# Optimization experiments

Measured on AMD Instinct MI355X. Metric: run time of the kernel, lower is better.

## Reference

```python
import jax, jax.numpy as jnp
import numpy as np

N_NODES = 100000
HIDDEN = 128
N_EDGES = 1600000


def setup_inputs() -> dict:
    key = jax.random.key(0)
    k_z, k_e, k_w1, k_b1, k_w2, k_b2 = jax.random.split(key, 6)
    z = jax.random.normal(k_z, (N_NODES, HIDDEN), dtype=jnp.float32)
    edge_index = jax.random.randint(k_e, (2, N_EDGES), 0, N_NODES, dtype=jnp.int64)
    # torch.nn.Linear default init: U(-1/sqrt(fan_in), 1/sqrt(fan_in))
    lim1 = 1.0 / np.sqrt(2 * HIDDEN)
    W1 = jax.random.uniform(k_w1, (2 * HIDDEN, HIDDEN), minval=-lim1, maxval=lim1, dtype=jnp.float32)
    b1 = jax.random.uniform(k_b1, (HIDDEN,), minval=-lim1, maxval=lim1, dtype=jnp.float32)
    lim2 = 1.0 / np.sqrt(HIDDEN)
    W2 = jax.random.uniform(k_w2, (HIDDEN, 1), minval=-lim2, maxval=lim2, dtype=jnp.float32)
    b2 = jax.random.uniform(k_b2, (1,), minval=-lim2, maxval=lim2, dtype=jnp.float32)
    return {"z": z, "edge_index": edge_index, "W1": W1, "b1": b1, "W2": W2, "b2": b2}


def reference(z, edge_index, W1, b1, W2, b2):
    src = edge_index[0]
    dst = edge_index[1]
    # gather node pairs -> concat: [E, 2H]
    edge_feat = jnp.concatenate([z[src], z[dst]], axis=1)
    h = jax.nn.relu(edge_feat @ W1 + b1)  # [E, H]
    score = h @ W2 + b2                   # [E, 1]
    return score
```

## Files before the change

kernel.cpp:

```cpp
#include <hip/hip_runtime.h>
#include <hip/hip_bf16.h>
#include <stdint.h>

#define HIDDEN 128

typedef __attribute__((ext_vector_type(8))) short bf16x8;
typedef __attribute__((ext_vector_type(16))) float f32x16;

static __device__ __forceinline__ unsigned short f2bf(float f) {
    union { float f; uint32_t u; } v; v.f = f;
    uint32_t u = v.u;
    uint32_t r = (u + 0x7fffu + ((u >> 16) & 1u)) >> 16;
    return (unsigned short)r;
}
static __device__ __forceinline__ float bf_lo(uint32_t p) {
    union { uint32_t u; float f; } v; v.u = p << 16; return v.f;
}
static __device__ __forceinline__ float bf_hi(uint32_t p) {
    union { uint32_t u; float f; } v; v.u = p & 0xffff0000u; return v.f;
}
static __device__ __forceinline__ bf16x8 pack8(float4 a, float4 b) {
    bf16x8 r;
    r[0] = (short)f2bf(a.x); r[1] = (short)f2bf(a.y);
    r[2] = (short)f2bf(a.z); r[3] = (short)f2bf(a.w);
    r[4] = (short)f2bf(b.x); r[5] = (short)f2bf(b.y);
    r[6] = (short)f2bf(b.z); r[7] = (short)f2bf(b.w);
    return r;
}


struct ZBuf { float4 a[8], b[8]; };

static __device__ __forceinline__ void load_z(ZBuf& zb, const float* __restrict__ z,
                                              int ng, int nl, int hi, int n_nodes) {
    int node = ng * 32 + nl;
    node = (node < n_nodes) ? node : (n_nodes - 1);
    const float* zrow = z + (size_t)node * HIDDEN;
    #pragma unroll
    for (int ks = 0; ks < 8; ++ks) {
        zb.a[ks] = *reinterpret_cast<const float4*>(zrow + ks * 16 + hi * 8);
        zb.b[ks] = *reinterpret_cast<const float4*>(zrow + ks * 16 + hi * 8 + 4);
    }
}

static __device__ __forceinline__ void compute_store(
    const ZBuf& zb, const bf16x8 (&wf)[2][8], const f32x16 (&binit)[2],
    unsigned short* __restrict__ UV, int ng, int nl, int hi, int w, int n_nodes)
{
    bf16x8 zf[8];
    #pragma unroll
    for (int ks = 0; ks < 8; ++ks) zf[ks] = pack8(zb.a[ks], zb.b[ks]);

    f32x16 acc0 = binit[0];
    f32x16 acc1 = binit[1];
    #pragma unroll
    for (int ks = 0; ks < 8; ++ks) {
        acc0 = __builtin_amdgcn_mfma_f32_32x32x16_bf16(wf[0][ks], zf[ks], acc0, 0, 0, 0);
        acc1 = __builtin_amdgcn_mfma_f32_32x32x16_bf16(wf[1][ks], zf[ks], acc1, 0, 0, 0);
    }

    const int node = ng * 32 + nl;
    if (node < n_nodes) {
        unsigned short* orow = UV + (size_t)node * 256;
        #pragma unroll
        for (int g = 0; g < 4; ++g) {
            ushort4 s0, s1;
            s0.x = f2bf(acc0[4 * g + 0]); s0.y = f2bf(acc0[4 * g + 1]);
            s0.z = f2bf(acc0[4 * g + 2]); s0.w = f2bf(acc0[4 * g + 3]);
            s1.x = f2bf(acc1[4 * g + 0]); s1.y = f2bf(acc1[4 * g + 1]);
            s1.z = f2bf(acc1[4 * g + 2]); s1.w = f2bf(acc1[4 * g + 3]);
            *reinterpret_cast<ushort4*>(orow + w * 64 + g * 8 + hi * 4) = s0;
            *reinterpret_cast<ushort4*>(orow + w * 64 + 32 + g * 8 + hi * 4) = s1;
        }
    }
}

__global__ __launch_bounds__(256) void precompute_mfma32(
    const float* __restrict__ z, const float* __restrict__ W1,
    const float* __restrict__ b1,
    unsigned short* __restrict__ UV, int n_nodes, int n_groups)
{
    const int lane = threadIdx.x & 63;
    const int w = threadIdx.x >> 6;
    const int nl = lane & 31;
    const int hi = lane >> 5;

    bf16x8 wf[2][8];
    #pragma unroll
    for (int cg = 0; cg < 2; ++cg) {
        const int cc = w * 64 + cg * 32 + nl;
        const int ccol = cc & 127;
        const int kofs = (cc >= 128) ? 128 : 0;
        #pragma unroll
        for (int ks = 0; ks < 8; ++ks) {
            const int k0 = ks * 16 + hi * 8 + kofs;
            bf16x8 f;
            #pragma unroll
            for (int j = 0; j < 8; ++j)
                f[j] = (short)f2bf(W1[(size_t)(k0 + j) * 128 + ccol]);
            wf[cg][ks] = f;
        }
    }

    f32x16 binit[2];
    #pragma unroll
    for (int cg = 0; cg < 2; ++cg) {
        const int cc0 = w * 64 + cg * 32;
        #pragma unroll
        for (int r = 0; r < 16; ++r) {
            const int crow = (r & 3) + 8 * (r >> 2) + 4 * hi;
            const int cc = cc0 + crow;
            binit[cg][r] = (cc < 128) ? b1[cc] : 0.f;
        }
    }

    const int stride = gridDim.x;
    int ng = blockIdx.x;
    if (ng >= n_groups) return;

    ZBuf bufA, bufB;
    load_z(bufA, z, ng, nl, hi, n_nodes);

    while (ng < n_groups) {
        const int n1 = ng + stride;
        if (n1 < n_groups) load_z(bufB, z, n1, nl, hi, n_nodes);
        compute_store(bufA, wf, binit, UV, ng, nl, hi, w, n_nodes);
        if (n1 >= n_groups) break;

        const int n2 = n1 + stride;
        if (n2 < n_groups) load_z(bufA, z, n2, nl, hi, n_nodes);
        compute_store(bufB, wf, binit, UV, n1, nl, hi, w, n_nodes);
        ng = n2;
    }
}

static __device__ __forceinline__ float dot8(uint4 u, uint4 v, const float* w) {
    const uint32_t up[4] = { u.x, u.y, u.z, u.w };
    const uint32_t vp[4] = { v.x, v.y, v.z, v.w };
    float s = 0.f;
    #pragma unroll
    for (int p = 0; p < 4; ++p) {
        const float h0 = bf_lo(up[p]) + bf_lo(vp[p]);
        const float h1 = bf_hi(up[p]) + bf_hi(vp[p]);
        s = fmaf(fmaxf(h0, 0.f), w[2 * p], s);
        s = fmaf(fmaxf(h1, 0.f), w[2 * p + 1], s);
    }
    return s;
}
static __device__ __forceinline__ float red16(float s) {
    s += __shfl_xor(s, 1, 64); s += __shfl_xor(s, 2, 64);
    s += __shfl_xor(s, 4, 64); s += __shfl_xor(s, 8, 64);
    return s;
}

#define EPG 12

__global__ __launch_bounds__(256) void edge_score(
    const int* __restrict__ ei, const unsigned short* __restrict__ UV,
    const float* __restrict__ W2, const float* __restrict__ b2,
    float* __restrict__ out, int n_edges)
{
    const int g = (blockIdx.x * 256 + threadIdx.x) >> 4;
    const int q = threadIdx.x & 15;
    const int e0 = g * EPG;
    if (e0 >= n_edges) return;

    const float4 w2a = *reinterpret_cast<const float4*>(W2 + q * 8);
    const float4 w2b = *reinterpret_cast<const float4*>(W2 + q * 8 + 4);
    const float wloc[8] = { w2a.x, w2a.y, w2a.z, w2a.w, w2b.x, w2b.y, w2b.z, w2b.w };
    const float bias = b2[0];

    const char* UVb = (const char*)UV;
    const uint32_t qo = (uint32_t)q * 16u;

    if (e0 + EPG - 1 < n_edges) {
        int sidx[EPG], didx[EPG];
        #pragma unroll
        for (int c = 0; c < EPG / 4; ++c) {
            const int4 s4 = *reinterpret_cast<const int4*>(ei + e0 + 4 * c);
            const int4 d4 = *reinterpret_cast<const int4*>(ei + n_edges + e0 + 4 * c);
            sidx[4 * c + 0] = s4.x; sidx[4 * c + 1] = s4.y;
            sidx[4 * c + 2] = s4.z; sidx[4 * c + 3] = s4.w;
            didx[4 * c + 0] = d4.x; didx[4 * c + 1] = d4.y;
            didx[4 * c + 2] = d4.z; didx[4 * c + 3] = d4.w;
        }

        uint4 u[EPG], v[EPG];
        #pragma unroll
        for (int i = 0; i < EPG; ++i) {
            u[i] = *reinterpret_cast<const uint4*>(UVb + ((uint32_t)sidx[i] * 512u + qo));
            v[i] = *reinterpret_cast<const uint4*>(UVb + ((uint32_t)didx[i] * 512u + 256u + qo));
        }

        float s[EPG];
        #pragma unroll
        for (int i = 0; i < EPG; ++i) s[i] = dot8(u[i], v[i], wloc);
        #pragma unroll
        for (int i = 0; i < EPG; ++i) s[i] = red16(s[i]) + bias;

        if (q == 0) {
            #pragma unroll
            for (int c = 0; c < EPG / 4; ++c) {
                float4 o = { s[4 * c], s[4 * c + 1], s[4 * c + 2], s[4 * c + 3] };
                *reinterpret_cast<float4*>(out + e0 + 4 * c) = o;
            }
        }
    } else {
        for (int i = 0; i < EPG; ++i) {
            const int e = e0 + i;
            if (e >= n_edges) break;
            const int si = ei[e];
            const int di = ei[n_edges + e];
            const uint4 uu = *reinterpret_cast<const uint4*>(UVb + ((uint32_t)si * 512u + qo));
            const uint4 vv = *reinterpret_cast<const uint4*>(UVb + ((uint32_t)di * 512u + 256u + qo));
            float s = red16(dot8(uu, vv, wloc));
            if (q == 0) out[e] = s + bias;
        }
    }
}

extern "C" void kernel_launch(void* const* d_in, const int* in_sizes, int n_in,
                              void* d_out, int out_size, void* d_ws, size_t ws_size,
                              hipStream_t stream) {
    const float* z  = (const float*)d_in[0];
    const int*   ei = (const int*)d_in[1];
    const float* W1 = (const float*)d_in[2];
    const float* b1 = (const float*)d_in[3];
    const float* W2 = (const float*)d_in[4];
    const float* b2 = (const float*)d_in[5];
    float* out = (float*)d_out;

    const int n_nodes = in_sizes[0] / HIDDEN;
    const int n_edges = in_sizes[1] / 2;

    unsigned short* UV = (unsigned short*)d_ws;

    {
        const int n_groups = (n_nodes + 31) / 32;
        const int g1 = n_groups < 512 ? n_groups : 512;
        precompute_mfma32<<<g1, 256, 0, stream>>>(z, W1, b1, UV, n_nodes, n_groups);
    }
    {
        const int groups = (n_edges + EPG - 1) / EPG;
        const int blocks = (groups * 16 + 255) / 256;
        edge_score<<<blocks, 256, 0, stream>>>(ei, UV, W2, b2, out, n_edges);
    }
}
```

Measured before the change: 155.2 us.

## Stage precompute output through swizzled LDS and retune edge kernel occupancy

The precompute kernel now writes MFMA results into a swizzled shared-memory tile and then copies full 512-byte rows to global memory with coalesced 16-byte stores, replacing scattered 8-byte stores. The edge-scoring kernel drops edges per group from 12 to 8, adds a launch-bounds occupancy hint, and puts a scheduling barrier after the gathers to keep loads batched. The LDS staging adds two block barriers per iteration, and the smaller edge batch means less memory-level parallelism per thread in exchange for more waves.

```diff
diff --git a/kernel.cpp b/kernel.cpp
--- a/kernel.cpp
+++ b/kernel.cpp
@@ -43,9 +43,9 @@
     }
 }
 
-static __device__ __forceinline__ void compute_store(
+static __device__ __forceinline__ void compute_to_lds(
     const ZBuf& zb, const bf16x8 (&wf)[2][8], const f32x16 (&binit)[2],
-    unsigned short* __restrict__ UV, int ng, int nl, int hi, int w, int n_nodes)
+    char* Sm, int nl, int hi, int w)
 {
     bf16x8 zf[8];
     #pragma unroll
@@ -59,18 +59,35 @@
         acc1 = __builtin_amdgcn_mfma_f32_32x32x16_bf16(wf[1][ks], zf[ks], acc1, 0, 0, 0);
     }
 
-    const int node = ng * 32 + nl;
-    if (node < n_nodes) {
-        unsigned short* orow = UV + (size_t)node * 256;
-        #pragma unroll
-        for (int g = 0; g < 4; ++g) {
-            ushort4 s0, s1;
-            s0.x = f2bf(acc0[4 * g + 0]); s0.y = f2bf(acc0[4 * g + 1]);
-            s0.z = f2bf(acc0[4 * g + 2]); s0.w = f2bf(acc0[4 * g + 3]);
-            s1.x = f2bf(acc1[4 * g + 0]); s1.y = f2bf(acc1[4 * g + 1]);
-            s1.z = f2bf(acc1[4 * g + 2]); s1.w = f2bf(acc1[4 * g + 3]);
-            *reinterpret_cast<ushort4*>(orow + w * 64 + g * 8 + hi * 4) = s0;
-            *reinterpret_cast<ushort4*>(orow + w * 64 + 32 + g * 8 + hi * 4) = s1;
+    const int swz = (nl & 15) << 3;
+    #pragma unroll
+    for (int g = 0; g < 4; ++g) {
+        ushort4 s0, s1;
+        s0.x = f2bf(acc0[4 * g + 0]); s0.y = f2bf(acc0[4 * g + 1]);
+        s0.z = f2bf(acc0[4 * g + 2]); s0.w = f2bf(acc0[4 * g + 3]);
+        s1.x = f2bf(acc1[4 * g + 0]); s1.y = f2bf(acc1[4 * g + 1]);
+        s1.z = f2bf(acc1[4 * g + 2]); s1.w = f2bf(acc1[4 * g + 3]);
+        const int colb0 = w * 128 + g * 16 + hi * 8;
+        const int colb1 = w * 128 + 64 + g * 16 + hi * 8;
+        *reinterpret_cast<ushort4*>(Sm + nl * 512 + (colb0 ^ swz)) = s0;
+        *reinterpret_cast<ushort4*>(Sm + nl * 512 + (colb1 ^ swz)) = s1;
+    }
+}
+
+static __device__ __forceinline__ void copy_out(
+    unsigned short* __restrict__ UV, const char* Sm, int ng, int tid, int n_nodes)
+{
+    const int colb0 = (tid & 31) * 16;
+    #pragma unroll
+    for (int rep = 0; rep < 4; ++rep) {
+        const int node_local = rep * 8 + (tid >> 5);
+        const int swz = (node_local & 15) << 3;
+        const uint2 g0 = *reinterpret_cast<const uint2*>(Sm + node_local * 512 + ((colb0) ^ swz));
+        const uint2 g1 = *reinterpret_cast<const uint2*>(Sm + node_local * 512 + ((colb0 + 8) ^ swz));
+        const int node = ng * 32 + node_local;
+        if (node < n_nodes) {
+            uint4 o = { g0.x, g0.y, g1.x, g1.y };
+            *reinterpret_cast<uint4*>(UV + (size_t)node * 256 + (tid & 31) * 8) = o;
         }
     }
 }
@@ -80,8 +97,11 @@
     const float* __restrict__ b1,
     unsigned short* __restrict__ UV, int n_nodes, int n_groups)
 {
-    const int lane = threadIdx.x & 63;
-    const int w = threadIdx.x >> 6;
+    __shared__ char Sm[32 * 512];
+
+    const int tid = threadIdx.x;
+    const int lane = tid & 63;
+    const int w = tid >> 6;
     const int nl = lane & 31;
     const int hi = lane >> 5;
 
@@ -124,12 +144,18 @@
     while (ng < n_groups) {
         const int n1 = ng + stride;
         if (n1 < n_groups) load_z(bufB, z, n1, nl, hi, n_nodes);
-        compute_store(bufA, wf, binit, UV, ng, nl, hi, w, n_nodes);
+        compute_to_lds(bufA, wf, binit, Sm, nl, hi, w);
+        __syncthreads();
+        copy_out(UV, Sm, ng, tid, n_nodes);
+        __syncthreads();
         if (n1 >= n_groups) break;
 
         const int n2 = n1 + stride;
         if (n2 < n_groups) load_z(bufA, z, n2, nl, hi, n_nodes);
-        compute_store(bufB, wf, binit, UV, n1, nl, hi, w, n_nodes);
+        compute_to_lds(bufB, wf, binit, Sm, nl, hi, w);
+        __syncthreads();
+        copy_out(UV, Sm, n1, tid, n_nodes);
+        __syncthreads();
         ng = n2;
     }
 }
@@ -153,9 +179,9 @@
     return s;
 }
 
-#define EPG 12
-
-__global__ __launch_bounds__(256) void edge_score(
+#define EPG 8
+
+__global__ __launch_bounds__(256, 4) void edge_score(
     const int* __restrict__ ei, const unsigned short* __restrict__ UV,
     const float* __restrict__ W2, const float* __restrict__ b2,
     float* __restrict__ out, int n_edges)
@@ -174,16 +200,12 @@
     const uint32_t qo = (uint32_t)q * 16u;
 
     if (e0 + EPG - 1 < n_edges) {
-        int sidx[EPG], didx[EPG];
-        #pragma unroll
-        for (int c = 0; c < EPG / 4; ++c) {
-            const int4 s4 = *reinterpret_cast<const int4*>(ei + e0 + 4 * c);
-            const int4 d4 = *reinterpret_cast<const int4*>(ei + n_edges + e0 + 4 * c);
-            sidx[4 * c + 0] = s4.x; sidx[4 * c + 1] = s4.y;
-            sidx[4 * c + 2] = s4.z; sidx[4 * c + 3] = s4.w;
-            didx[4 * c + 0] = d4.x; didx[4 * c + 1] = d4.y;
-            didx[4 * c + 2] = d4.z; didx[4 * c + 3] = d4.w;
-        }
+        const int4 sA = *reinterpret_cast<const int4*>(ei + e0);
+        const int4 sB = *reinterpret_cast<const int4*>(ei + e0 + 4);
+        const int4 dA = *reinterpret_cast<const int4*>(ei + n_edges + e0);
+        const int4 dB = *reinterpret_cast<const int4*>(ei + n_edges + e0 + 4);
+        const int sidx[EPG] = { sA.x, sA.y, sA.z, sA.w, sB.x, sB.y, sB.z, sB.w };
+        const int didx[EPG] = { dA.x, dA.y, dA.z, dA.w, dB.x, dB.y, dB.z, dB.w };
 
         uint4 u[EPG], v[EPG];
         #pragma unroll
@@ -191,6 +213,7 @@
             u[i] = *reinterpret_cast<const uint4*>(UVb + ((uint32_t)sidx[i] * 512u + qo));
             v[i] = *reinterpret_cast<const uint4*>(UVb + ((uint32_t)didx[i] * 512u + 256u + qo));
         }
+        __builtin_amdgcn_sched_barrier(0);
 
         float s[EPG];
         #pragma unroll
@@ -199,11 +222,10 @@
         for (int i = 0; i < EPG; ++i) s[i] = red16(s[i]) + bias;
 
         if (q == 0) {
-            #pragma unroll
-            for (int c = 0; c < EPG / 4; ++c) {
-                float4 o = { s[4 * c], s[4 * c + 1], s[4 * c + 2], s[4 * c + 3] };
-                *reinterpret_cast<float4*>(out + e0 + 4 * c) = o;
-            }
+            float4 oA = { s[0], s[1], s[2], s[3] };
+            float4 oB = { s[4], s[5], s[6], s[7] };
+            *reinterpret_cast<float4*>(out + e0) = oA;
+            *reinterpret_cast<float4*>(out + e0 + 4) = oB;
         }
     } else {
         for (int i = 0; i < EPG; ++i) {
```

New measurement: 149.1 us. 1.04x faster.
